# Performance work log

Measured on AMD Instinct MI355X. Metric: run time of the kernel, lower is better.

Reference implementation:

```python
import jax, jax.numpy as jnp
import numpy as np

S, L = 4096, 12
VOCAB, CHARS, TAGS = 100000, 128, 64
CE, CH, WE, H = 64, 128, 256, 512


def setup_inputs() -> dict:
    key = jax.random.key(0)
    ks = jax.random.split(key, 16)
    n = lambda k, shp, s=0.05: (jax.random.normal(k, shp, jnp.float32) * s)
    return {
        "w_seq": jax.random.randint(ks[0], (S,), 0, VOCAB),
        "c_seq": jax.random.randint(ks[1], (S, L), 0, CHARS),
        "char_emb": n(ks[2], (CHARS, CE), 1.0),
        "word_emb": n(ks[3], (VOCAB, WE), 1.0),
        "c_hx0": jnp.zeros((CH,), jnp.float32),
        "c_cx0": jnp.zeros((CH,), jnp.float32),
        "hx0": jnp.zeros((H,), jnp.float32),
        "cx0": jnp.zeros((H,), jnp.float32),
        "Wih1": n(ks[4], (4 * CH, CE)),
        "Whh1": n(ks[5], (4 * CH, CH)),
        "bih1": n(ks[6], (4 * CH,)),
        "bhh1": n(ks[7], (4 * CH,)),
        "Wih2": n(ks[8], (4 * H, WE + CH)),
        "Whh2": n(ks[9], (4 * H, H)),
        "bih2": n(ks[10], (4 * H,)),
        "bhh2": n(ks[11], (4 * H,)),
        "W_out": n(ks[12], (TAGS, H)),
        "b_out": n(ks[13], (TAGS,)),
    }


def _lstm_step(x, h, c, Wih, Whh, b):
    # PyTorch gate order: i, f, g, o
    g = x @ Wih.T + h @ Whh.T + b
    i, f, gg, o = jnp.split(g, 4, axis=-1)
    c = jax.nn.sigmoid(f) * c + jax.nn.sigmoid(i) * jnp.tanh(gg)
    h = jax.nn.sigmoid(o) * jnp.tanh(c)
    return h, c


def reference(w_seq, c_seq, char_emb, word_emb, c_hx0, c_cx0, hx0, cx0,
              Wih1, Whh1, bih1, bhh1, Wih2, Whh2, bih2, bhh2, W_out, b_out):
    nwords = w_seq.shape[0]
    # --- batched per-word char LSTM (all words run as one batch) ---
    xs = jnp.transpose(char_emb[c_seq], (1, 0, 2))  # [L, S, CE]
    b1 = bih1 + bhh1
    h0 = jnp.broadcast_to(c_hx0, (nwords, c_hx0.shape[0]))
    c0 = jnp.broadcast_to(c_cx0, (nwords, c_cx0.shape[0]))

    def step1(carry, x):
        h, c = _lstm_step(x, carry[0], carry[1], Wih1, Whh1, b1)
        return (h, c), None

    (char_rep, _), _ = jax.lax.scan(step1, (h0, c0), xs)  # [S, CH]

    # --- word-level LSTM over the sentence ---
    wv = word_emb[w_seq]                                  # [S, WE]
    seq = jnp.concatenate([char_rep, wv], axis=1)         # [S, CH+WE]
    b2 = bih2 + bhh2

    def step2(carry, x):
        h, c = _lstm_step(x, carry[0], carry[1], Wih2, Whh2, b2)
        return (h, c), h

    _, outs = jax.lax.scan(step2, (hx0, cx0), seq)        # [S, H]

    tag_space = outs @ W_out.T + b_out                    # [S, TAGS]
    return jax.nn.log_softmax(tag_space, axis=1)
```

## Files before the change

kernel.cpp:

```cpp
#include <hip/hip_runtime.h>
#include <math.h>

#define S_LEN 4096
#define L_CH  12
#define CE    64
#define CHD   128
#define WE    256
#define HD    512
#define TAGS  64
#define GW    (4*HD)
#define XDIM  (CHD+WE)
#define NBLK  32

#define WS_GX    0
#define WS_CREP  (WS_GX   + (size_t)S_LEN*GW)
#define WS_HEXT  (WS_CREP + (size_t)S_LEN*CHD)

typedef float v4f __attribute__((ext_vector_type(4)));

static __device__ __forceinline__ float sigf(float x) {
    return 1.0f / (1.0f + __expf(-x));
}
static __device__ __forceinline__ float tanhfast(float x) {
    return 1.0f - 2.0f / (__expf(2.0f * x) + 1.0f);
}
static __device__ __forceinline__ float dot4(v4f a, v4f b) {
    return a.x*b.x + a.y*b.y + a.z*b.z + a.w*b.w;
}
template <int CTRL, int RMASK>
static __device__ __forceinline__ float dpp_add(float a) {
    int t = __builtin_amdgcn_update_dpp(0, __float_as_int(a), CTRL, RMASK, 0xf, true);
    return a + __int_as_float(t);
}
static __device__ __forceinline__ float rdlane(float v, int l) {
    return __int_as_float(__builtin_amdgcn_readlane(__float_as_int(v), l));
}

__global__ __launch_bounds__(256) void k_init(const float* __restrict__ hx0,
                                              float* __restrict__ hext) {
    size_t i = ((size_t)blockIdx.x * 256 + threadIdx.x) * 4;
    if (i >= (size_t)(S_LEN + 1) * HD) return;
    v4f v;
    if (i < HD) {
        v.x = hx0[i+0] + 2.0f; v.y = hx0[i+1] + 2.0f;
        v.z = hx0[i+2] + 2.0f; v.w = hx0[i+3] + 2.0f;
    } else {
        v.x = 0.f; v.y = 0.f; v.z = 0.f; v.w = 0.f;
    }
    float* p = hext + i;
    asm volatile("global_store_dwordx4 %0, %1, off sc0 sc1"
                 :: "v"(p), "v"(v) : "memory");
}

__global__ __launch_bounds__(256) void k_char_lstm(
    const int* __restrict__ c_seq, const float* __restrict__ char_emb,
    const float* __restrict__ c_hx0, const float* __restrict__ c_cx0,
    const float* __restrict__ Wih1, const float* __restrict__ Whh1,
    const float* __restrict__ bih1, const float* __restrict__ bhh1,
    float* __restrict__ char_rep)
{
    __shared__ float xs[16][CE + 4];
    __shared__ float hs[16][CHD + 4];
    __shared__ float cs[16][CHD + 4];
    __shared__ float gs[16][4*CHD + 4];
    const int tid = threadIdx.x;
    const int w0  = blockIdx.x * 16;

    for (int u = tid; u < 16*CHD; u += 256) {
        int w = u >> 7, k = u & (CHD-1);
        hs[w][k] = c_hx0[k];
        cs[w][k] = c_cx0[k];
    }
    __syncthreads();

    const int wg = tid & 3;
    const int rg = tid >> 2;
    const int uw = tid >> 4;
    const int uj = (tid & 15) * 8;

    for (int t = 0; t < L_CH; ++t) {
        {
            int w = tid >> 4, k4 = (tid & 15) * 4;
            int ci = c_seq[(w0 + w) * L_CH + t];
            float4 v = *(const float4*)(char_emb + (size_t)ci * CE + k4);
            *(float4*)&xs[w][k4] = v;
        }
        __syncthreads();

        float acc[8][4];
        #pragma unroll
        for (int i = 0; i < 8; ++i)
            #pragma unroll
            for (int j = 0; j < 4; ++j) acc[i][j] = 0.0f;

        for (int kc = 0; kc < CE/4; ++kc) {
            int k = kc * 4;
            float4 xv[4];
            #pragma unroll
            for (int j = 0; j < 4; ++j) xv[j] = *(const float4*)&xs[wg*4 + j][k];
            #pragma unroll
            for (int i = 0; i < 8; ++i) {
                int r = rg*8 + i;
                float4 wv = *(const float4*)(Wih1 + (size_t)r*CE + k);
                #pragma unroll
                for (int j = 0; j < 4; ++j)
                    acc[i][j] += wv.x*xv[j].x + wv.y*xv[j].y + wv.z*xv[j].z + wv.w*xv[j].w;
            }
        }
        for (int kc = 0; kc < CHD/4; ++kc) {
            int k = kc * 4;
            float4 hv[4];
            #pragma unroll
            for (int j = 0; j < 4; ++j) hv[j] = *(const float4*)&hs[wg*4 + j][k];
            #pragma unroll
            for (int i = 0; i < 8; ++i) {
                int r = rg*8 + i;
                float4 wv = *(const float4*)(Whh1 + (size_t)r*CHD + k);
                #pragma unroll
                for (int j = 0; j < 4; ++j)
                    acc[i][j] += wv.x*hv[j].x + wv.y*hv[j].y + wv.z*hv[j].z + wv.w*hv[j].w;
            }
        }
        #pragma unroll
        for (int i = 0; i < 8; ++i) {
            int r = rg*8 + i;
            float b = bih1[r] + bhh1[r];
            #pragma unroll
            for (int j = 0; j < 4; ++j) gs[wg*4 + j][r] = acc[i][j] + b;
        }
        __syncthreads();

        #pragma unroll
        for (int i = 0; i < 8; ++i) {
            int j = uj + i;
            float gi = gs[uw][j];
            float gf = gs[uw][CHD + j];
            float gg = gs[uw][2*CHD + j];
            float go = gs[uw][3*CHD + j];
            float c = sigf(gf)*cs[uw][j] + sigf(gi)*tanhfast(gg);
            cs[uw][j] = c;
            hs[uw][j] = sigf(go)*tanhfast(c);
        }
        __syncthreads();
    }
    #pragma unroll
    for (int i4 = 0; i4 < 2; ++i4) {
        float4 v;
        v.x = hs[uw][uj + i4*4 + 0]; v.y = hs[uw][uj + i4*4 + 1];
        v.z = hs[uw][uj + i4*4 + 2]; v.w = hs[uw][uj + i4*4 + 3];
        *(float4*)(char_rep + (size_t)(w0 + uw)*CHD + uj + i4*4) = v;
    }
}

__global__ __launch_bounds__(256) void k_gx(
    const int* __restrict__ w_seq, const float* __restrict__ word_emb,
    const float* __restrict__ char_rep,
    const float* __restrict__ Wih2, const float* __restrict__ bih2,
    const float* __restrict__ bhh2, float* __restrict__ Gx)
{
    __shared__ float xs[16][XDIM + 4];
    const int tid = threadIdx.x;
    const int w0  = blockIdx.x * 16;
    const int slice = blockIdx.y;

    {
        int w = tid >> 4, seg = tid & 15;
        int wsq = w_seq[w0 + w];
        #pragma unroll
        for (int i4 = 0; i4 < 6; ++i4) {
            int k = seg*24 + i4*4;
            float4 v;
            if (k < CHD) v = *(const float4*)(char_rep + (size_t)(w0+w)*CHD + k);
            else         v = *(const float4*)(word_emb + (size_t)wsq*WE + (k - CHD));
            *(float4*)&xs[w][k] = v;
        }
    }
    __syncthreads();

    const int wg = tid & 3, rg = tid >> 2;
    float acc[8][4];
    #pragma unroll
    for (int i = 0; i < 8; ++i)
        #pragma unroll
        for (int j = 0; j < 4; ++j) acc[i][j] = 0.0f;

    for (int kc = 0; kc < XDIM/4; ++kc) {
        int k = kc * 4;
        float4 xv[4];
        #pragma unroll
        for (int j = 0; j < 4; ++j) xv[j] = *(const float4*)&xs[wg*4 + j][k];
        #pragma unroll
        for (int i = 0; i < 8; ++i) {
            int r = slice*512 + rg*8 + i;
            float4 wv = *(const float4*)(Wih2 + (size_t)r*XDIM + k);
            #pragma unroll
            for (int j = 0; j < 4; ++j)
                acc[i][j] += wv.x*xv[j].x + wv.y*xv[j].y + wv.z*xv[j].z + wv.w*xv[j].w;
        }
    }
    #pragma unroll
    for (int i = 0; i < 8; ++i) {
        int r = slice*512 + rg*8 + i;
        float b = bih2[r] + bhh2[r];
        #pragma unroll
        for (int j = 0; j < 4; ++j)
            Gx[(size_t)(w0 + wg*4 + j)*GW + r] = acc[i][j] + b;
    }
}

__global__ __launch_bounds__(256, 1) void k_word_lstm(
    const float* __restrict__ Gx, const float* __restrict__ Whh2,
    const float* __restrict__ cx0, float* __restrict__ hext)
{
    __shared__ __align__(16) float hsh[2][16];
    const int tid  = threadIdx.x;
    const int w    = tid >> 6;
    const int lane = tid & 63;
    const int jb   = blockIdx.x * 16;
    const int jo4  = jb + w * 4;
    const int g2   = lane >> 5;
    const int qe   = g2 * 2, qo = qe + 1;
    const int kk   = (lane & 31) * 16;

    v4f we_[4][4], wo_[4][4];
    float wse[4], wso[4];
    #pragma unroll
    for (int o = 0; o < 4; ++o) {
        const float* pe = Whh2 + (size_t)(qe*HD + jo4 + o)*HD + kk;
        const float* po = Whh2 + (size_t)(qo*HD + jo4 + o)*HD + kk;
        asm volatile(
            "global_load_dwordx4 %0, %8, off\n\t"
            "global_load_dwordx4 %1, %8, off offset:16\n\t"
            "global_load_dwordx4 %2, %8, off offset:32\n\t"
            "global_load_dwordx4 %3, %8, off offset:48\n\t"
            "global_load_dwordx4 %4, %9, off\n\t"
            "global_load_dwordx4 %5, %9, off offset:16\n\t"
            "global_load_dwordx4 %6, %9, off offset:32\n\t"
            "global_load_dwordx4 %7, %9, off offset:48\n\t"
            "s_waitcnt vmcnt(0)"
            : "=&v"(we_[o][0]), "=&v"(we_[o][1]), "=&v"(we_[o][2]), "=&v"(we_[o][3]),
              "=&v"(wo_[o][0]), "=&v"(wo_[o][1]), "=&v"(wo_[o][2]), "=&v"(wo_[o][3])
            : "v"(pe), "v"(po));
        wse[o] = 2.0f * (we_[o][0].x+we_[o][0].y+we_[o][0].z+we_[o][0].w
                       + we_[o][1].x+we_[o][1].y+we_[o][1].z+we_[o][1].w
                       + we_[o][2].x+we_[o][2].y+we_[o][2].z+we_[o][2].w
                       + we_[o][3].x+we_[o][3].y+we_[o][3].z+we_[o][3].w);
        wso[o] = 2.0f * (wo_[o][0].x+wo_[o][0].y+wo_[o][0].z+wo_[o][0].w
                       + wo_[o][1].x+wo_[o][1].y+wo_[o][1].z+wo_[o][1].w
                       + wo_[o][2].x+wo_[o][2].y+wo_[o][2].z+wo_[o][2].w
                       + wo_[o][3].x+wo_[o][3].y+wo_[o][3].z+wo_[o][3].w);
    }

    float creg[4];
    #pragma unroll
    for (int o = 0; o < 4; ++o) creg[o] = cx0[jo4 + o];

    for (int t = 0; t < S_LEN; ++t) {
        const float* gp = Gx + (size_t)t*GW + jo4;
        float gxa[4][4];
        {
            float4 v0 = *(const float4*)(gp);
            float4 v1 = *(const float4*)(gp + HD);
            float4 v2 = *(const float4*)(gp + 2*HD);
            float4 v3 = *(const float4*)(gp + 3*HD);
            gxa[0][0]=v0.x; gxa[0][1]=v0.y; gxa[0][2]=v0.z; gxa[0][3]=v0.w;
            gxa[1][0]=v1.x; gxa[1][1]=v1.y; gxa[1][2]=v1.z; gxa[1][3]=v1.w;
            gxa[2][0]=v2.x; gxa[2][1]=v2.y; gxa[2][2]=v2.z; gxa[2][3]=v2.w;
            gxa[3][0]=v3.x; gxa[3][1]=v3.y; gxa[3][2]=v3.z; gxa[3][3]=v3.w;
        }

        const float* hsrc = hext + (size_t)t*HD + kk;
        v4f r0, r1, r2, r3;
        for (;;) {
            asm volatile(
                "global_load_dwordx4 %0, %4, off sc0 sc1\n\t"
                "global_load_dwordx4 %1, %4, off offset:16 sc0 sc1\n\t"
                "global_load_dwordx4 %2, %4, off offset:32 sc0 sc1\n\t"
                "global_load_dwordx4 %3, %4, off offset:48 sc0 sc1\n\t"
                "s_waitcnt vmcnt(0)"
                : "=&v"(r0), "=&v"(r1), "=&v"(r2), "=&v"(r3)
                : "v"(hsrc)
                : "memory");
            float mn = fminf(fminf(fminf(r0.x, r0.y), fminf(r0.z, r0.w)),
                             fminf(fminf(r1.x, r1.y), fminf(r1.z, r1.w)));
            mn = fminf(mn, fminf(fminf(fminf(r2.x, r2.y), fminf(r2.z, r2.w)),
                                 fminf(fminf(r3.x, r3.y), fminf(r3.z, r3.w))));
            if (__all(mn > 0.5f)) break;
        }

        float ae[4], ao[4];
        #pragma unroll
        for (int o = 0; o < 4; ++o) {
            ae[o] = dot4(we_[o][0], r0) + dot4(we_[o][1], r1)
                  + dot4(we_[o][2], r2) + dot4(we_[o][3], r3) - wse[o];
            ao[o] = dot4(wo_[o][0], r0) + dot4(wo_[o][1], r1)
                  + dot4(wo_[o][2], r2) + dot4(wo_[o][3], r3) - wso[o];
        }

        #pragma unroll
        for (int o = 0; o < 4; ++o) {
            ae[o] = dpp_add<0x111, 0xf>(ae[o]); ao[o] = dpp_add<0x111, 0xf>(ao[o]);
            ae[o] = dpp_add<0x112, 0xf>(ae[o]); ao[o] = dpp_add<0x112, 0xf>(ao[o]);
            ae[o] = dpp_add<0x114, 0xf>(ae[o]); ao[o] = dpp_add<0x114, 0xf>(ao[o]);
            ae[o] = dpp_add<0x118, 0xf>(ae[o]); ao[o] = dpp_add<0x118, 0xf>(ao[o]);
            ae[o] = dpp_add<0x142, 0xa>(ae[o]); ao[o] = dpp_add<0x142, 0xa>(ao[o]);
        }

        float hn[4];
        #pragma unroll
        for (int o = 0; o < 4; ++o) {
            float si = rdlane(ae[o], 31), sf = rdlane(ao[o], 31);
            float sg = rdlane(ae[o], 63), so = rdlane(ao[o], 63);
            float g0 = gxa[0][o] + si;
            float g1 = gxa[1][o] + sf;
            float g2v = gxa[2][o] + sg;
            float g3 = gxa[3][o] + so;
            float c  = sigf(g1)*creg[o] + sigf(g0)*tanhfast(g2v);
            creg[o] = c;
            hn[o] = sigf(g3)*tanhfast(c) + 2.0f;
        }

        if (lane == 0) {
            float4 hv; hv.x = hn[0]; hv.y = hn[1]; hv.z = hn[2]; hv.w = hn[3];
            *(float4*)&hsh[t & 1][w*4] = hv;
        }
        __syncthreads();
        if (tid < 16) {
            float v = hsh[t & 1][tid];
            float* dst = hext + (size_t)(t+1)*HD + jb + tid;
            asm volatile("global_store_dword %0, %1, off sc0 sc1"
                         :: "v"(dst), "v"(v) : "memory");
        }
    }
}

__global__ __launch_bounds__(256) void k_out(
    const float* __restrict__ outs_b, const float* __restrict__ W_out,
    const float* __restrict__ b_out, float* __restrict__ out)
{
    __shared__ float hh[16][HD + 4];
    __shared__ float ts[16][TAGS + 4];
    __shared__ float lse[16];
    const int tid = threadIdx.x;
    const int w0  = blockIdx.x * 16;

    {
        int w = tid >> 4, k0 = (tid & 15) * 32;
        #pragma unroll
        for (int i4 = 0; i4 < 8; ++i4) {
            float4 v = *(const float4*)(outs_b + (size_t)(w0+w)*HD + k0 + i4*4);
            int k = k0 + i4*4;
            hh[w][k+0] = v.x - 2.0f; hh[w][k+1] = v.y - 2.0f;
            hh[w][k+2] = v.z - 2.0f; hh[w][k+3] = v.w - 2.0f;
        }
    }
    __syncthreads();

    const int tag = tid & 63;
    const int wg  = tid >> 6;
    float a0 = 0.f, a1 = 0.f, a2 = 0.f, a3 = 0.f;
    for (int kc = 0; kc < HD/4; ++kc) {
        int k = kc * 4;
        float4 wv = *(const float4*)(W_out + (size_t)tag*HD + k);
        float4 x0 = *(const float4*)&hh[wg*4+0][k];
        float4 x1 = *(const float4*)&hh[wg*4+1][k];
        float4 x2 = *(const float4*)&hh[wg*4+2][k];
        float4 x3 = *(const float4*)&hh[wg*4+3][k];
        a0 += wv.x*x0.x + wv.y*x0.y + wv.z*x0.z + wv.w*x0.w;
        a1 += wv.x*x1.x + wv.y*x1.y + wv.z*x1.z + wv.w*x1.w;
        a2 += wv.x*x2.x + wv.y*x2.y + wv.z*x2.z + wv.w*x2.w;
        a3 += wv.x*x3.x + wv.y*x3.y + wv.z*x3.z + wv.w*x3.w;
    }
    float bo = b_out[tag];
    ts[wg*4+0][tag] = a0 + bo;
    ts[wg*4+1][tag] = a1 + bo;
    ts[wg*4+2][tag] = a2 + bo;
    ts[wg*4+3][tag] = a3 + bo;
    __syncthreads();

    if (tid < 16) {
        float m = -1e30f;
        for (int q = 0; q < TAGS; ++q) m = fmaxf(m, ts[tid][q]);
        float ssum = 0.0f;
        for (int q = 0; q < TAGS; ++q) ssum += __expf(ts[tid][q] - m);
        lse[tid] = m + __logf(ssum);
    }
    __syncthreads();

    #pragma unroll
    for (int jjj = 0; jjj < 4; ++jjj)
        out[(size_t)(w0 + wg*4 + jjj)*TAGS + tag] = ts[wg*4+jjj][tag] - lse[wg*4+jjj];
}

extern "C" void kernel_launch(void* const* d_in, const int* in_sizes, int n_in,
                              void* d_out, int out_size, void* d_ws, size_t ws_size,
                              hipStream_t stream) {
    (void)in_sizes; (void)n_in; (void)out_size; (void)ws_size;
    const int*   w_seq    = (const int*)  d_in[0];
    const int*   c_seq    = (const int*)  d_in[1];
    const float* char_emb = (const float*)d_in[2];
    const float* word_emb = (const float*)d_in[3];
    const float* c_hx0    = (const float*)d_in[4];
    const float* c_cx0    = (const float*)d_in[5];
    const float* hx0      = (const float*)d_in[6];
    const float* cx0      = (const float*)d_in[7];
    const float* Wih1     = (const float*)d_in[8];
    const float* Whh1     = (const float*)d_in[9];
    const float* bih1     = (const float*)d_in[10];
    const float* bhh1     = (const float*)d_in[11];
    const float* Wih2     = (const float*)d_in[12];
    const float* Whh2     = (const float*)d_in[13];
    const float* bih2     = (const float*)d_in[14];
    const float* bhh2     = (const float*)d_in[15];
    const float* W_out    = (const float*)d_in[16];
    const float* b_out    = (const float*)d_in[17];

    float* ws   = (float*)d_ws;
    float* Gx   = ws + WS_GX;
    float* crep = ws + WS_CREP;
    float* hext = ws + WS_HEXT;

    int init_blocks = (int)(((size_t)(S_LEN + 1) * HD / 4 + 255) / 256);
    hipLaunchKernelGGL(k_init, dim3(init_blocks), dim3(256), 0, stream, hx0, hext);
    hipLaunchKernelGGL(k_char_lstm, dim3(256), dim3(256), 0, stream,
                       c_seq, char_emb, c_hx0, c_cx0, Wih1, Whh1, bih1, bhh1, crep);
    hipLaunchKernelGGL(k_gx, dim3(256, 4), dim3(256), 0, stream,
                       w_seq, word_emb, crep, Wih2, bih2, bhh2, Gx);
    hipLaunchKernelGGL(k_word_lstm, dim3(NBLK), dim3(256), 0, stream,
                       Gx, Whh2, cx0, hext);
    hipLaunchKernelGGL(k_out, dim3(256), dim3(256), 0, stream,
                       hext + HD, W_out, b_out, (float*)d_out);
}
```

Baseline: 10.99 ms.

## Co-locate word LSTM blocks on one XCD and exchange hidden state via L2 ring

Launches 256 word-LSTM blocks and elects the first 32 that land on the same XCD (read from the XCC_ID hardware register) to do the recurrence, while the rest exit. Each step's hidden state is also written to a two-slot ring buffer with sc0-only stores and polled without sc1, so inter-block exchange can stay in the shared XCD L2 instead of going through system-coherent memory. Stale versus fresh ring values are told apart by alternating value-range offsets. The old hext path remains as a fallback poll on later iterations. This relies on the scheduler placing 32 blocks on one XCD, and the election spin adds startup latency.

```diff
diff --git a/kernel.cpp b/kernel.cpp
--- a/kernel.cpp
+++ b/kernel.cpp
@@ -10,11 +10,13 @@
 #define TAGS  64
 #define GW    (4*HD)
 #define XDIM  (CHD+WE)
-#define NBLK  32
+#define WL_GRID 256
 
 #define WS_GX    0
 #define WS_CREP  (WS_GX   + (size_t)S_LEN*GW)
 #define WS_HEXT  (WS_CREP + (size_t)S_LEN*CHD)
+#define WS_RING  (WS_HEXT + (size_t)(S_LEN+1)*HD)
+#define WS_CTRL  (WS_RING + (size_t)2*HD)
 
 typedef float v4f __attribute__((ext_vector_type(4)));
 
@@ -37,19 +39,39 @@
 }
 
 __global__ __launch_bounds__(256) void k_init(const float* __restrict__ hx0,
-                                              float* __restrict__ hext) {
-    size_t i = ((size_t)blockIdx.x * 256 + threadIdx.x) * 4;
-    if (i >= (size_t)(S_LEN + 1) * HD) return;
-    v4f v;
-    if (i < HD) {
-        v.x = hx0[i+0] + 2.0f; v.y = hx0[i+1] + 2.0f;
-        v.z = hx0[i+2] + 2.0f; v.w = hx0[i+3] + 2.0f;
-    } else {
-        v.x = 0.f; v.y = 0.f; v.z = 0.f; v.w = 0.f;
-    }
-    float* p = hext + i;
-    asm volatile("global_store_dwordx4 %0, %1, off sc0 sc1"
-                 :: "v"(p), "v"(v) : "memory");
+                                              float* __restrict__ hext,
+                                              float* __restrict__ ring,
+                                              int* __restrict__ ctrl) {
+    const int tid = threadIdx.x;
+    size_t i = ((size_t)blockIdx.x * 256 + tid) * 4;
+    if (i < (size_t)(S_LEN + 1) * HD) {
+        v4f v;
+        if (i < HD) {
+            v.x = hx0[i+0] + 2.0f; v.y = hx0[i+1] + 2.0f;
+            v.z = hx0[i+2] + 2.0f; v.w = hx0[i+3] + 2.0f;
+        } else {
+            v.x = 0.f; v.y = 0.f; v.z = 0.f; v.w = 0.f;
+        }
+        float* p = hext + i;
+        asm volatile("global_store_dwordx4 %0, %1, off sc0 sc1"
+                     :: "v"(p), "v"(v) : "memory");
+    }
+    if (blockIdx.x == 0) {
+        if (tid < 9) ctrl[tid] = 0;
+        if (tid < 128) {
+            int k = tid * 4;
+            v4f a;
+            a.x = hx0[k+0] + 2.0f; a.y = hx0[k+1] + 2.0f;
+            a.z = hx0[k+2] + 2.0f; a.w = hx0[k+3] + 2.0f;
+            v4f z; z.x = 0.f; z.y = 0.f; z.z = 0.f; z.w = 0.f;
+            float* p0 = ring + k;
+            float* p1 = ring + HD + k;
+            asm volatile("global_store_dwordx4 %0, %1, off sc0 sc1"
+                         :: "v"(p0), "v"(a) : "memory");
+            asm volatile("global_store_dwordx4 %0, %1, off sc0 sc1"
+                         :: "v"(p1), "v"(z) : "memory");
+        }
+    }
 }
 
 __global__ __launch_bounds__(256) void k_char_lstm(
@@ -210,13 +232,38 @@
 
 __global__ __launch_bounds__(256, 1) void k_word_lstm(
     const float* __restrict__ Gx, const float* __restrict__ Whh2,
-    const float* __restrict__ cx0, float* __restrict__ hext)
+    const float* __restrict__ cx0, float* __restrict__ hext,
+    float* __restrict__ ring, int* __restrict__ ctrl)
 {
     __shared__ __align__(16) float hsh[2][16];
+    __shared__ int sslot;
     const int tid  = threadIdx.x;
+
+    unsigned int xcd;
+    asm volatile("s_getreg_b32 %0, hwreg(HW_REG_XCC_ID)" : "=s"(xcd));
+    xcd &= 7u;
+    if (tid == 0) {
+        int slot = atomicAdd(&ctrl[xcd], 1);
+        int mine = -1;
+        if (slot < 32) {
+            if (slot == 31) atomicCAS(&ctrl[8], 0, (int)xcd + 1);
+            int ch;
+            do {
+                __builtin_amdgcn_s_sleep(8);
+                ch = __hip_atomic_load(&ctrl[8], __ATOMIC_RELAXED,
+                                       __HIP_MEMORY_SCOPE_AGENT);
+            } while (ch == 0);
+            if (ch == (int)xcd + 1) mine = slot;
+        }
+        sslot = mine;
+    }
+    __syncthreads();
+    const int slot = sslot;
+    if (slot < 0) return;
+
     const int w    = tid >> 6;
     const int lane = tid & 63;
-    const int jb   = blockIdx.x * 16;
+    const int jb   = slot * 16;
     const int jo4  = jb + w * 4;
     const int g2   = lane >> 5;
     const int qe   = g2 * 2, qo = qe + 1;
@@ -241,14 +288,14 @@
             : "=&v"(we_[o][0]), "=&v"(we_[o][1]), "=&v"(we_[o][2]), "=&v"(we_[o][3]),
               "=&v"(wo_[o][0]), "=&v"(wo_[o][1]), "=&v"(wo_[o][2]), "=&v"(wo_[o][3])
             : "v"(pe), "v"(po));
-        wse[o] = 2.0f * (we_[o][0].x+we_[o][0].y+we_[o][0].z+we_[o][0].w
-                       + we_[o][1].x+we_[o][1].y+we_[o][1].z+we_[o][1].w
-                       + we_[o][2].x+we_[o][2].y+we_[o][2].z+we_[o][2].w
-                       + we_[o][3].x+we_[o][3].y+we_[o][3].z+we_[o][3].w);
-        wso[o] = 2.0f * (wo_[o][0].x+wo_[o][0].y+wo_[o][0].z+wo_[o][0].w
-                       + wo_[o][1].x+wo_[o][1].y+wo_[o][1].z+wo_[o][1].w
-                       + wo_[o][2].x+wo_[o][2].y+wo_[o][2].z+wo_[o][2].w
-                       + wo_[o][3].x+wo_[o][3].y+wo_[o][3].z+wo_[o][3].w);
+        wse[o] = we_[o][0].x+we_[o][0].y+we_[o][0].z+we_[o][0].w
+               + we_[o][1].x+we_[o][1].y+we_[o][1].z+we_[o][1].w
+               + we_[o][2].x+we_[o][2].y+we_[o][2].z+we_[o][2].w
+               + we_[o][3].x+we_[o][3].y+we_[o][3].z+we_[o][3].w;
+        wso[o] = wo_[o][0].x+wo_[o][0].y+wo_[o][0].z+wo_[o][0].w
+               + wo_[o][1].x+wo_[o][1].y+wo_[o][1].z+wo_[o][1].w
+               + wo_[o][2].x+wo_[o][2].y+wo_[o][2].z+wo_[o][2].w
+               + wo_[o][3].x+wo_[o][3].y+wo_[o][3].z+wo_[o][3].w;
     }
 
     float creg[4];
@@ -269,32 +316,61 @@
             gxa[3][0]=v3.x; gxa[3][1]=v3.y; gxa[3][2]=v3.z; gxa[3][3]=v3.w;
         }
 
+        const int   ebt  = (t >> 1) & 1;
+        const float lo   = 0.5f + 4.0f * (float)ebt;
+        const float hi   = 3.5f + 4.0f * (float)ebt;
+        const float* rsrc = ring + (size_t)(t & 1)*HD + kk;
         const float* hsrc = hext + (size_t)t*HD + kk;
         v4f r0, r1, r2, r3;
-        for (;;) {
-            asm volatile(
-                "global_load_dwordx4 %0, %4, off sc0 sc1\n\t"
-                "global_load_dwordx4 %1, %4, off offset:16 sc0 sc1\n\t"
-                "global_load_dwordx4 %2, %4, off offset:32 sc0 sc1\n\t"
-                "global_load_dwordx4 %3, %4, off offset:48 sc0 sc1\n\t"
-                "s_waitcnt vmcnt(0)"
-                : "=&v"(r0), "=&v"(r1), "=&v"(r2), "=&v"(r3)
-                : "v"(hsrc)
-                : "memory");
-            float mn = fminf(fminf(fminf(r0.x, r0.y), fminf(r0.z, r0.w)),
-                             fminf(fminf(r1.x, r1.y), fminf(r1.z, r1.w)));
-            mn = fminf(mn, fminf(fminf(fminf(r2.x, r2.y), fminf(r2.z, r2.w)),
-                                 fminf(fminf(r3.x, r3.y), fminf(r3.z, r3.w))));
-            if (__all(mn > 0.5f)) break;
+        float bias = 2.0f;
+        for (int it = 0; ; ++it) {
+            if (it >= 6 && (it & 1)) {
+                asm volatile(
+                    "global_load_dwordx4 %0, %4, off sc0 sc1\n\t"
+                    "global_load_dwordx4 %1, %4, off offset:16 sc0 sc1\n\t"
+                    "global_load_dwordx4 %2, %4, off offset:32 sc0 sc1\n\t"
+                    "global_load_dwordx4 %3, %4, off offset:48 sc0 sc1\n\t"
+                    "s_waitcnt vmcnt(0)"
+                    : "=&v"(r0), "=&v"(r1), "=&v"(r2), "=&v"(r3)
+                    : "v"(hsrc)
+                    : "memory");
+                float mn = fminf(fminf(fminf(r0.x, r0.y), fminf(r0.z, r0.w)),
+                                 fminf(fminf(r1.x, r1.y), fminf(r1.z, r1.w)));
+                mn = fminf(mn, fminf(fminf(fminf(r2.x, r2.y), fminf(r2.z, r2.w)),
+                                     fminf(fminf(r3.x, r3.y), fminf(r3.z, r3.w))));
+                if (__all(mn > 0.5f)) { bias = 2.0f; break; }
+            } else {
+                asm volatile(
+                    "global_load_dwordx4 %0, %4, off sc0\n\t"
+                    "global_load_dwordx4 %1, %4, off offset:16 sc0\n\t"
+                    "global_load_dwordx4 %2, %4, off offset:32 sc0\n\t"
+                    "global_load_dwordx4 %3, %4, off offset:48 sc0\n\t"
+                    "s_waitcnt vmcnt(0)"
+                    : "=&v"(r0), "=&v"(r1), "=&v"(r2), "=&v"(r3)
+                    : "v"(rsrc)
+                    : "memory");
+                float mn = fminf(fminf(fminf(r0.x, r0.y), fminf(r0.z, r0.w)),
+                                 fminf(fminf(r1.x, r1.y), fminf(r1.z, r1.w)));
+                mn = fminf(mn, fminf(fminf(fminf(r2.x, r2.y), fminf(r2.z, r2.w)),
+                                     fminf(fminf(r3.x, r3.y), fminf(r3.z, r3.w))));
+                float mx = fmaxf(fmaxf(fmaxf(r0.x, r0.y), fmaxf(r0.z, r0.w)),
+                                 fmaxf(fmaxf(r1.x, r1.y), fmaxf(r1.z, r1.w)));
+                mx = fmaxf(mx, fmaxf(fmaxf(fmaxf(r2.x, r2.y), fmaxf(r2.z, r2.w)),
+                                     fmaxf(fmaxf(r3.x, r3.y), fmaxf(r3.z, r3.w))));
+                if (__all((mn > lo) && (mx < hi))) {
+                    bias = 2.0f + 4.0f * (float)ebt;
+                    break;
+                }
+            }
         }
 
         float ae[4], ao[4];
         #pragma unroll
         for (int o = 0; o < 4; ++o) {
             ae[o] = dot4(we_[o][0], r0) + dot4(we_[o][1], r1)
-                  + dot4(we_[o][2], r2) + dot4(we_[o][3], r3) - wse[o];
+                  + dot4(we_[o][2], r2) + dot4(we_[o][3], r3) - bias*wse[o];
             ao[o] = dot4(wo_[o][0], r0) + dot4(wo_[o][1], r1)
-                  + dot4(wo_[o][2], r2) + dot4(wo_[o][3], r3) - wso[o];
+                  + dot4(wo_[o][2], r2) + dot4(wo_[o][3], r3) - bias*wso[o];
         }
 
         #pragma unroll
@@ -320,7 +396,14 @@
             hn[o] = sigf(g3)*tanhfast(c) + 2.0f;
         }
 
+        const float eb4n = 4.0f * (float)(((t + 1) >> 1) & 1);
         if (lane == 0) {
+            v4f rv;
+            rv.x = hn[0] + eb4n; rv.y = hn[1] + eb4n;
+            rv.z = hn[2] + eb4n; rv.w = hn[3] + eb4n;
+            float* rdst = ring + (size_t)((t + 1) & 1)*HD + jo4;
+            asm volatile("global_store_dwordx4 %0, %1, off sc0"
+                         :: "v"(rdst), "v"(rv) : "memory");
             float4 hv; hv.x = hn[0]; hv.y = hn[1]; hv.z = hn[2]; hv.w = hn[3];
             *(float4*)&hsh[t & 1][w*4] = hv;
         }
@@ -419,15 +502,18 @@
     float* Gx   = ws + WS_GX;
     float* crep = ws + WS_CREP;
     float* hext = ws + WS_HEXT;
+    float* ring = ws + WS_RING;
+    int*   ctrl = (int*)(ws + WS_CTRL);
 
     int init_blocks = (int)(((size_t)(S_LEN + 1) * HD / 4 + 255) / 256);
-    hipLaunchKernelGGL(k_init, dim3(init_blocks), dim3(256), 0, stream, hx0, hext);
+    hipLaunchKernelGGL(k_init, dim3(init_blocks), dim3(256), 0, stream,
+                       hx0, hext, ring, ctrl);
     hipLaunchKernelGGL(k_char_lstm, dim3(256), dim3(256), 0, stream,
                        c_seq, char_emb, c_hx0, c_cx0, Wih1, Whh1, bih1, bhh1, crep);
     hipLaunchKernelGGL(k_gx, dim3(256, 4), dim3(256), 0, stream,
                        w_seq, word_emb, crep, Wih2, bih2, bhh2, Gx);
-    hipLaunchKernelGGL(k_word_lstm, dim3(NBLK), dim3(256), 0, stream,
-                       Gx, Whh2, cx0, hext);
+    hipLaunchKernelGGL(k_word_lstm, dim3(WL_GRID), dim3(256), 0, stream,
+                       Gx, Whh2, cx0, hext, ring, ctrl);
     hipLaunchKernelGGL(k_out, dim3(256), dim3(256), 0, stream,
                        hext + HD, W_out, b_out, (float*)d_out);
 }
```

Result: slower. 13.33 ms (+21.3%).

## Split h polling across warps via LDS, prefetch next Gx, store h directly

Applied to the files above, without the earlier changes.

In the word-LSTM recurrence, each wavefront now polls only a quarter of the published hidden state (one dwordx4 per lane instead of four). The pieces are shared through double-buffered LDS behind a block barrier, so each lane no longer spins on its full 16-float slice. Gx for step t+1 is prefetched into registers during step t. Each wave's lane 0 stores its four h values straight to global memory with a dwordx4, which drops the second barrier. The aim is to cut global polling traffic and latency on the serial critical path, at the cost of one barrier per step whose timing depends on the slowest-polling wave.

```diff
diff --git a/kernel.cpp b/kernel.cpp
--- a/kernel.cpp
+++ b/kernel.cpp
@@ -212,7 +212,7 @@
     const float* __restrict__ Gx, const float* __restrict__ Whh2,
     const float* __restrict__ cx0, float* __restrict__ hext)
 {
-    __shared__ __align__(16) float hsh[2][16];
+    __shared__ float hsh[2][HD];
     const int tid  = threadIdx.x;
     const int w    = tid >> 6;
     const int lane = tid & 63;
@@ -221,6 +221,7 @@
     const int g2   = lane >> 5;
     const int qe   = g2 * 2, qo = qe + 1;
     const int kk   = (lane & 31) * 16;
+    const int pq   = w * 128 + (lane & 31) * 4;
 
     v4f we_[4][4], wo_[4][4];
     float wse[4], wso[4];
@@ -241,60 +242,67 @@
             : "=&v"(we_[o][0]), "=&v"(we_[o][1]), "=&v"(we_[o][2]), "=&v"(we_[o][3]),
               "=&v"(wo_[o][0]), "=&v"(wo_[o][1]), "=&v"(wo_[o][2]), "=&v"(wo_[o][3])
             : "v"(pe), "v"(po));
-        wse[o] = 2.0f * (we_[o][0].x+we_[o][0].y+we_[o][0].z+we_[o][0].w
-                       + we_[o][1].x+we_[o][1].y+we_[o][1].z+we_[o][1].w
-                       + we_[o][2].x+we_[o][2].y+we_[o][2].z+we_[o][2].w
-                       + we_[o][3].x+we_[o][3].y+we_[o][3].z+we_[o][3].w);
-        wso[o] = 2.0f * (wo_[o][0].x+wo_[o][0].y+wo_[o][0].z+wo_[o][0].w
-                       + wo_[o][1].x+wo_[o][1].y+wo_[o][1].z+wo_[o][1].w
-                       + wo_[o][2].x+wo_[o][2].y+wo_[o][2].z+wo_[o][2].w
-                       + wo_[o][3].x+wo_[o][3].y+wo_[o][3].z+wo_[o][3].w);
+        wse[o] = we_[o][0].x+we_[o][0].y+we_[o][0].z+we_[o][0].w
+               + we_[o][1].x+we_[o][1].y+we_[o][1].z+we_[o][1].w
+               + we_[o][2].x+we_[o][2].y+we_[o][2].z+we_[o][2].w
+               + we_[o][3].x+we_[o][3].y+we_[o][3].z+we_[o][3].w;
+        wso[o] = wo_[o][0].x+wo_[o][0].y+wo_[o][0].z+wo_[o][0].w
+               + wo_[o][1].x+wo_[o][1].y+wo_[o][1].z+wo_[o][1].w
+               + wo_[o][2].x+wo_[o][2].y+wo_[o][2].z+wo_[o][2].w
+               + wo_[o][3].x+wo_[o][3].y+wo_[o][3].z+wo_[o][3].w;
     }
 
     float creg[4];
     #pragma unroll
     for (int o = 0; o < 4; ++o) creg[o] = cx0[jo4 + o];
 
+    float4 cu0, cu1, cu2, cu3;
+    {
+        const float* gp = Gx + jo4;
+        cu0 = *(const float4*)(gp);
+        cu1 = *(const float4*)(gp + HD);
+        cu2 = *(const float4*)(gp + 2*HD);
+        cu3 = *(const float4*)(gp + 3*HD);
+    }
+
     for (int t = 0; t < S_LEN; ++t) {
-        const float* gp = Gx + (size_t)t*GW + jo4;
-        float gxa[4][4];
+        float4 nx0, nx1, nx2, nx3;
         {
-            float4 v0 = *(const float4*)(gp);
-            float4 v1 = *(const float4*)(gp + HD);
-            float4 v2 = *(const float4*)(gp + 2*HD);
-            float4 v3 = *(const float4*)(gp + 3*HD);
-            gxa[0][0]=v0.x; gxa[0][1]=v0.y; gxa[0][2]=v0.z; gxa[0][3]=v0.w;
-            gxa[1][0]=v1.x; gxa[1][1]=v1.y; gxa[1][2]=v1.z; gxa[1][3]=v1.w;
-            gxa[2][0]=v2.x; gxa[2][1]=v2.y; gxa[2][2]=v2.z; gxa[2][3]=v2.w;
-            gxa[3][0]=v3.x; gxa[3][1]=v3.y; gxa[3][2]=v3.z; gxa[3][3]=v3.w;
-        }
-
-        const float* hsrc = hext + (size_t)t*HD + kk;
-        v4f r0, r1, r2, r3;
+            int tn = (t + 1 < S_LEN) ? t + 1 : t;
+            const float* gp = Gx + (size_t)tn*GW + jo4;
+            nx0 = *(const float4*)(gp);
+            nx1 = *(const float4*)(gp + HD);
+            nx2 = *(const float4*)(gp + 2*HD);
+            nx3 = *(const float4*)(gp + 3*HD);
+        }
+
+        const float* psrc = hext + (size_t)t*HD + pq;
+        v4f pr;
         for (;;) {
             asm volatile(
-                "global_load_dwordx4 %0, %4, off sc0 sc1\n\t"
-                "global_load_dwordx4 %1, %4, off offset:16 sc0 sc1\n\t"
-                "global_load_dwordx4 %2, %4, off offset:32 sc0 sc1\n\t"
-                "global_load_dwordx4 %3, %4, off offset:48 sc0 sc1\n\t"
+                "global_load_dwordx4 %0, %1, off sc0 sc1\n\t"
                 "s_waitcnt vmcnt(0)"
-                : "=&v"(r0), "=&v"(r1), "=&v"(r2), "=&v"(r3)
-                : "v"(hsrc)
+                : "=&v"(pr)
+                : "v"(psrc)
                 : "memory");
-            float mn = fminf(fminf(fminf(r0.x, r0.y), fminf(r0.z, r0.w)),
-                             fminf(fminf(r1.x, r1.y), fminf(r1.z, r1.w)));
-            mn = fminf(mn, fminf(fminf(fminf(r2.x, r2.y), fminf(r2.z, r2.w)),
-                                 fminf(fminf(r3.x, r3.y), fminf(r3.z, r3.w))));
+            float mn = fminf(fminf(pr.x, pr.y), fminf(pr.z, pr.w));
             if (__all(mn > 0.5f)) break;
         }
+        if (lane < 32) *(v4f*)&hsh[t & 1][pq] = pr;
+        __syncthreads();
+
+        v4f r0 = *(const v4f*)&hsh[t & 1][kk + 0];
+        v4f r1 = *(const v4f*)&hsh[t & 1][kk + 4];
+        v4f r2 = *(const v4f*)&hsh[t & 1][kk + 8];
+        v4f r3 = *(const v4f*)&hsh[t & 1][kk + 12];
 
         float ae[4], ao[4];
         #pragma unroll
         for (int o = 0; o < 4; ++o) {
             ae[o] = dot4(we_[o][0], r0) + dot4(we_[o][1], r1)
-                  + dot4(we_[o][2], r2) + dot4(we_[o][3], r3) - wse[o];
+                  + dot4(we_[o][2], r2) + dot4(we_[o][3], r3) - 2.0f*wse[o];
             ao[o] = dot4(wo_[o][0], r0) + dot4(wo_[o][1], r1)
-                  + dot4(wo_[o][2], r2) + dot4(wo_[o][3], r3) - wso[o];
+                  + dot4(wo_[o][2], r2) + dot4(wo_[o][3], r3) - 2.0f*wso[o];
         }
 
         #pragma unroll
@@ -311,26 +319,23 @@
         for (int o = 0; o < 4; ++o) {
             float si = rdlane(ae[o], 31), sf = rdlane(ao[o], 31);
             float sg = rdlane(ae[o], 63), so = rdlane(ao[o], 63);
-            float g0 = gxa[0][o] + si;
-            float g1 = gxa[1][o] + sf;
-            float g2v = gxa[2][o] + sg;
-            float g3 = gxa[3][o] + so;
+            float g0 = cu0[o] + si;
+            float g1 = cu1[o] + sf;
+            float g2v = cu2[o] + sg;
+            float g3 = cu3[o] + so;
             float c  = sigf(g1)*creg[o] + sigf(g0)*tanhfast(g2v);
             creg[o] = c;
             hn[o] = sigf(g3)*tanhfast(c) + 2.0f;
         }
 
         if (lane == 0) {
-            float4 hv; hv.x = hn[0]; hv.y = hn[1]; hv.z = hn[2]; hv.w = hn[3];
-            *(float4*)&hsh[t & 1][w*4] = hv;
-        }
-        __syncthreads();
-        if (tid < 16) {
-            float v = hsh[t & 1][tid];
-            float* dst = hext + (size_t)(t+1)*HD + jb + tid;
-            asm volatile("global_store_dword %0, %1, off sc0 sc1"
-                         :: "v"(dst), "v"(v) : "memory");
-        }
+            v4f hv; hv.x = hn[0]; hv.y = hn[1]; hv.z = hn[2]; hv.w = hn[3];
+            float* hdst = hext + (size_t)(t+1)*HD + jo4;
+            asm volatile("global_store_dwordx4 %0, %1, off sc0 sc1"
+                         :: "v"(hdst), "v"(hv) : "memory");
+        }
+
+        cu0 = nx0; cu1 = nx1; cu2 = nx2; cu3 = nx3;
     }
 }
 
```

New measurement: 11.72 ms. +6.6%, slower.
